# Optimization experiments

Hardware: AMD Instinct MI355X
Metric: run time of the kernel (lower is better)

Reference implementation:

```python
import jax, jax.numpy as jnp
import numpy as np

N_NODES = 100000
N_EDGES = 1600000
HIDDEN = 64
EPS = 1e-5


def setup_inputs() -> dict:
    key = jax.random.key(0)
    ks = jax.random.split(key, 12)
    h = HIDDEN
    inp = {
        'x': jax.random.normal(ks[0], (N_NODES, h), dtype=jnp.float32),
        'edge_index': jax.random.randint(ks[1], (2, N_EDGES), 0, N_NODES, dtype=jnp.int32),
        'message': jax.random.normal(ks[2], (N_EDGES, h), dtype=jnp.float32),
        # node_mlp: Linear(2h->h), BN(h), ReLU, Dropout(identity), Linear(h->h), BN(h), ReLU
        'W1': jax.random.normal(ks[3], (2 * h, h), dtype=jnp.float32) / np.sqrt(2.0 * h),
        'b1': jnp.zeros((h,), jnp.float32),
        'g1': jnp.ones((h,), jnp.float32),
        'be1': jnp.zeros((h,), jnp.float32),
        'W2': jax.random.normal(ks[4], (h, h), dtype=jnp.float32) / np.sqrt(h),
        'b2': jnp.zeros((h,), jnp.float32),
        'g2': jnp.ones((h,), jnp.float32),
        'be2': jnp.zeros((h,), jnp.float32),
        # attention_mlp: Linear(h->1), Sigmoid
        'Wa': jax.random.normal(ks[5], (h, 1), dtype=jnp.float32) / np.sqrt(h),
        'ba': jnp.zeros((1,), jnp.float32),
    }
    return inp


def _scatter_max(msg, idx, n):
    # torch_scatter scatter(..., reduce='max') fills segments with no edges with 0
    agg = jax.ops.segment_max(msg, idx, num_segments=n)  # [N, H], -inf where empty
    cnt = jax.ops.segment_sum(jnp.ones((idx.shape[0],), msg.dtype), idx, num_segments=n)
    return jnp.where(cnt[:, None] > 0, agg, jnp.zeros((), msg.dtype))


def _batchnorm(x, gamma, beta):
    # training-mode BatchNorm1d: batch mean / biased variance
    mu = jnp.mean(x, axis=0)
    var = jnp.mean((x - mu) ** 2, axis=0)
    return (x - mu) * jax.lax.rsqrt(var + EPS) * gamma + beta


def reference(x, edge_index, message, W1, b1, g1, be1, W2, b2, g2, be2, Wa, ba):
    n = x.shape[0]
    row, col = edge_index[0], edge_index[1]
    fwd = _scatter_max(message, col, n)   # [N, H]
    bwd = _scatter_max(message, row, n)   # [N, H]
    out = jnp.concatenate([fwd, bwd], axis=1)          # [N, 2H]
    h1 = jax.nn.relu(_batchnorm(out @ W1 + b1, g1, be1))  # dropout = identity (eval)
    h2 = jax.nn.relu(_batchnorm(h1 @ W2 + b2, g2, be2))   # [N, H]
    att = jax.nn.sigmoid(h2 @ Wa + ba).reshape(-1)          # [N]
    return (h2, att)
```

## Files before the change

kernel.cpp:

```cpp
#include <hip/hip_runtime.h>
#include <hip/hip_bf16.h>
#include <cstdint>
#include <cstddef>

#define HDIM 64
#define EPS 1e-5f
#define BN 64
#define BSH 6
#define LR 65
#define NXCD 8
#define BCAPX 256
#define SENTE 64u

typedef short bf16x8 __attribute__((ext_vector_type(8)));
typedef float f32x4  __attribute__((ext_vector_type(4)));
typedef float f4v    __attribute__((ext_vector_type(4)));
typedef unsigned u2v __attribute__((ext_vector_type(2)));

__device__ __forceinline__ unsigned bf16rn(float f) {
    unsigned u = __float_as_uint(f);
    return (u + 0x7FFFu + ((u >> 16) & 1u)) >> 16;
}

__global__ __launch_bounds__(256) void bucket_fill_kernel(
    const int* __restrict__ ei, unsigned* __restrict__ bcur,
    unsigned* __restrict__ entries, int E, int nblk) {
    int e = blockIdx.x * 256 + threadIdx.x;
    if (e >= E) return;
    unsigned xcd;
    asm volatile("s_getreg_b32 %0, hwreg(HW_REG_XCC_ID)" : "=s"(xcd));
    xcd &= (NXCD - 1);
    int row = ei[e];
    int col = ei[(size_t)E + e];
    unsigned cell1 = (unsigned)(col >> BSH) * NXCD + xcd;
    unsigned p1 = atomicAdd(&bcur[cell1], 1u);
    if (p1 < BCAPX)
        entries[(size_t)cell1 * BCAPX + p1] = ((unsigned)e << 7) | (unsigned)(col & (BN - 1));
    unsigned cell2 = (unsigned)(nblk + (row >> BSH)) * NXCD + xcd;
    unsigned p2 = atomicAdd(&bcur[cell2], 1u);
    if (p2 < BCAPX)
        entries[(size_t)cell2 * BCAPX + p2] = ((unsigned)e << 7) | (unsigned)(row & (BN - 1));
}

__global__ __launch_bounds__(256) void binned_max_kernel(
    const float* __restrict__ msg, const unsigned* __restrict__ bcur,
    const unsigned* __restrict__ entries,
    unsigned short* __restrict__ fwdB, unsigned short* __restrict__ bwdB,
    int N, int nblk) {
    __shared__ __align__(16) float acc[4 * LR * BN];
    int tid = threadIdx.x;
    int wave = tid >> 6, lane = tid & 63;
    int b = blockIdx.x;

    {
        f4v mi = { -INFINITY, -INFINITY, -INFINITY, -INFINITY };
        f4v* p = (f4v*)acc;
        for (int i = tid; i < 4 * LR * BN / 4; i += 256) p[i] = mi;
    }
    __syncthreads();
    float* accw = acc + wave * (LR * BN);

    for (int rr = 0; rr < 2; ++rr) {
        int r = wave + rr * 4;
        unsigned cnt = bcur[(size_t)b * NXCD + r];
        if (cnt > BCAPX) cnt = BCAPX;
        const unsigned* rb = entries + ((size_t)b * NXCD + r) * BCAPX;
        for (unsigned c0 = 0; c0 < cnt; c0 += 64) {
            unsigned myent = (c0 + (unsigned)lane < cnt) ? rb[c0 + lane] : SENTE;
            unsigned rem = cnt - c0;
#pragma unroll
            for (int b16 = 0; b16 < 4; ++b16) {
                if ((unsigned)(b16 * 16) >= rem) break;
                float v[16]; unsigned sl[16];
#pragma unroll
                for (int k = 0; k < 16; ++k) {
                    unsigned ent = __shfl(myent, b16 * 16 + k);
                    sl[k] = ent & 127u;
                    v[k] = __builtin_nontemporal_load(&msg[(size_t)(ent >> 7) * HDIM + lane]);
                }
#pragma unroll
                for (int k = 0; k < 16; ++k) {
                    float* a = &accw[sl[k] * BN + lane];
                    *a = fmaxf(*a, v[k]);
                }
            }
        }
    }
    __syncthreads();

    bool fwd = (b < nblk);
    int node0 = (fwd ? b : b - nblk) * BN;
    unsigned short* dst = fwd ? fwdB : bwdB;
    for (int i = tid; i < BN * (HDIM / 4); i += 256) {
        int rrow = i >> 4, c4 = (i & 15) * 4;
        int node = node0 + rrow;
        if (node >= N) continue;
        int off = rrow * HDIM + c4;
        f4v m0 = *(const f4v*)&acc[0 * LR * BN + off];
        f4v m1 = *(const f4v*)&acc[1 * LR * BN + off];
        f4v m2 = *(const f4v*)&acc[2 * LR * BN + off];
        f4v m3 = *(const f4v*)&acc[3 * LR * BN + off];
        f4v m;
#pragma unroll
        for (int k = 0; k < 4; ++k) {
            float x = fmaxf(fmaxf(m0[k], m1[k]), fmaxf(m2[k], m3[k]));
            m[k] = (x == -INFINITY) ? 0.0f : x;
        }
        u2v o;
        o.x = bf16rn(m[0]) | (bf16rn(m[1]) << 16);
        o.y = bf16rn(m[2]) | (bf16rn(m[3]) << 16);
        *(u2v*)(dst + (size_t)node * HDIM + c4) = o;
    }
}


__global__ __launch_bounds__(256) void prep_w_kernel(
    const float* __restrict__ W1, const float* __restrict__ W2,
    unsigned short* __restrict__ W1T, unsigned short* __restrict__ W2T) {
    int t = blockIdx.x * 256 + threadIdx.x;
    if (t < 128 * 64) {
        int k = t >> 6, o = t & 63;
        W1T[o * 128 + k] = (unsigned short)bf16rn(W1[t]);
    } else {
        int t2 = t - 128 * 64;
        if (t2 < 64 * 64) {
            int k = t2 >> 6, o = t2 & 63;
            W2T[o * 64 + k] = (unsigned short)bf16rn(W2[t2]);
        }
    }
}

__global__ __launch_bounds__(256) void gemm1_mfma_kernel(
    const unsigned short* __restrict__ fwdB, const unsigned short* __restrict__ bwdB,
    const unsigned short* __restrict__ W1T, const float* __restrict__ b1,
    float* __restrict__ y1, float* __restrict__ sum1, float* __restrict__ sq1, int N) {
    __shared__ float wsum[4][64], wsq[4][64];
    int tid = threadIdx.x;
    int wave = tid >> 6, lane = tid & 63;
    int lrow = lane & 15, kseg = lane >> 4;
    int rbase = blockIdx.x * 64 + wave * 16;

    bf16x8 bfr[4][4];
#pragma unroll
    for (int nt = 0; nt < 4; ++nt)
#pragma unroll
        for (int kb = 0; kb < 4; ++kb)
            bfr[nt][kb] = *(const bf16x8*)(W1T + (size_t)(nt * 16 + lrow) * 128 + kb * 32 + kseg * 8);

    int r = rbase + lrow;
    bool ok = (r < N);
    size_t ro = (size_t)(ok ? r : 0) * HDIM;
    bf16x8 z = {};
    bf16x8 afr[4];
    afr[0] = *(const bf16x8*)(fwdB + ro + kseg * 8);
    afr[1] = *(const bf16x8*)(fwdB + ro + 32 + kseg * 8);
    afr[2] = *(const bf16x8*)(bwdB + ro + kseg * 8);
    afr[3] = *(const bf16x8*)(bwdB + ro + 32 + kseg * 8);
    if (!ok) { afr[0] = z; afr[1] = z; afr[2] = z; afr[3] = z; }

    f32x4 acc[4] = {};
#pragma unroll
    for (int kb = 0; kb < 4; ++kb)
#pragma unroll
        for (int nt = 0; nt < 4; ++nt)
            acc[nt] = __builtin_amdgcn_mfma_f32_16x16x32_bf16(afr[kb], bfr[nt][kb], acc[nt], 0, 0, 0);

#pragma unroll
    for (int nt = 0; nt < 4; ++nt) {
        int col = nt * 16 + lrow;
        float bias = b1[col];
        float s = 0.f, q = 0.f;
#pragma unroll
        for (int rr = 0; rr < 4; ++rr) {
            int rowi = rbase + kseg * 4 + rr;
            if (rowi < N) {
                float v = acc[nt][rr] + bias;
                y1[(size_t)rowi * HDIM + col] = v;
                s += v; q += v * v;
            }
        }
        s += __shfl_xor(s, 16); s += __shfl_xor(s, 32);
        q += __shfl_xor(q, 16); q += __shfl_xor(q, 32);
        if (kseg == 0) { wsum[wave][col] = s; wsq[wave][col] = q; }
    }
    __syncthreads();
    if (tid < 64) {
        float S = wsum[0][tid] + wsum[1][tid] + wsum[2][tid] + wsum[3][tid];
        float Q = wsq[0][tid] + wsq[1][tid] + wsq[2][tid] + wsq[3][tid];
        atomicAdd(&sum1[tid], S);
        atomicAdd(&sq1[tid], Q);
    }
}

__global__ __launch_bounds__(256) void gemm2_mfma_kernel(
    const float* __restrict__ y1, const float* __restrict__ sum1, const float* __restrict__ sq1,
    const float* __restrict__ g1, const float* __restrict__ be1,
    const unsigned short* __restrict__ W2T, const float* __restrict__ b2,
    float* __restrict__ y2, float* __restrict__ sum2, float* __restrict__ sq2, int N) {
    __shared__ float sc[64], sh[64];
    __shared__ float wsum[4][64], wsq[4][64];
    int tid = threadIdx.x;
    if (tid < 64) {
        float invN = 1.0f / (float)N;
        float mu = sum1[tid] * invN;
        float var = sq1[tid] * invN - mu * mu;
        float rs = rsqrtf(var + EPS);
        float s = rs * g1[tid];
        sc[tid] = s;
        sh[tid] = be1[tid] - mu * s;
    }
    __syncthreads();
    int wave = tid >> 6, lane = tid & 63;
    int lrow = lane & 15, kseg = lane >> 4;
    int rbase = blockIdx.x * 64 + wave * 16;

    bf16x8 bfr[4][2];
#pragma unroll
    for (int nt = 0; nt < 4; ++nt)
#pragma unroll
        for (int kb = 0; kb < 2; ++kb)
            bfr[nt][kb] = *(const bf16x8*)(W2T + (size_t)(nt * 16 + lrow) * 64 + kb * 32 + kseg * 8);

    int r = rbase + lrow;
    size_t ro = (size_t)((r < N) ? r : 0) * HDIM;
    bf16x8 afr[2];
#pragma unroll
    for (int kb = 0; kb < 2; ++kb) {
        const f4v* yp = (const f4v*)(y1 + ro + kb * 32 + kseg * 8);
        f4v u0 = yp[0], u1 = yp[1];
        int k0 = kb * 32 + kseg * 8;
        bf16x8 a;
#pragma unroll
        for (int j = 0; j < 4; ++j) {
            float h0 = fmaxf(fmaf(u0[j], sc[k0 + j], sh[k0 + j]), 0.f);
            float h1 = fmaxf(fmaf(u1[j], sc[k0 + 4 + j], sh[k0 + 4 + j]), 0.f);
            a[j] = (short)bf16rn(h0);
            a[4 + j] = (short)bf16rn(h1);
        }
        afr[kb] = a;
    }

    f32x4 acc[4] = {};
#pragma unroll
    for (int kb = 0; kb < 2; ++kb)
#pragma unroll
        for (int nt = 0; nt < 4; ++nt)
            acc[nt] = __builtin_amdgcn_mfma_f32_16x16x32_bf16(afr[kb], bfr[nt][kb], acc[nt], 0, 0, 0);

#pragma unroll
    for (int nt = 0; nt < 4; ++nt) {
        int col = nt * 16 + lrow;
        float bias = b2[col];
        float s = 0.f, q = 0.f;
#pragma unroll
        for (int rr = 0; rr < 4; ++rr) {
            int rowi = rbase + kseg * 4 + rr;
            if (rowi < N) {
                float v = acc[nt][rr] + bias;
                y2[(size_t)rowi * HDIM + col] = v;
                s += v; q += v * v;
            }
        }
        s += __shfl_xor(s, 16); s += __shfl_xor(s, 32);
        q += __shfl_xor(q, 16); q += __shfl_xor(q, 32);
        if (kseg == 0) { wsum[wave][col] = s; wsq[wave][col] = q; }
    }
    __syncthreads();
    if (tid < 64) {
        float S = wsum[0][tid] + wsum[1][tid] + wsum[2][tid] + wsum[3][tid];
        float Q = wsq[0][tid] + wsq[1][tid] + wsq[2][tid] + wsq[3][tid];
        atomicAdd(&sum2[tid], S);
        atomicAdd(&sq2[tid], Q);
    }
}

__global__ __launch_bounds__(256) void final_kernel(
    const float* __restrict__ y2, const float* __restrict__ sum2, const float* __restrict__ sq2,
    const float* __restrict__ g2, const float* __restrict__ be2,
    const float* __restrict__ Wa, const float* __restrict__ ba,
    float* __restrict__ out_h2, float* __restrict__ out_att, int N) {
    __shared__ float sc[HDIM], sh[HDIM], wa[HDIM];
    __shared__ float bav;
    if (threadIdx.x < HDIM) {
        int c = threadIdx.x;
        float invN = 1.0f / (float)N;
        float mu = sum2[c] * invN;
        float var = sq2[c] * invN - mu * mu;
        float rstd = rsqrtf(var + EPS);
        float s = rstd * g2[c];
        sc[c] = s;
        sh[c] = be2[c] - mu * s;
        wa[c] = Wa[c];
    }
    if (threadIdx.x == 0) bav = ba[0];
    __syncthreads();
    int n = blockIdx.x * 256 + threadIdx.x;
    if (n >= N) return;

    const f4v* p = (const f4v*)&y2[(size_t)n * HDIM];
    f4v* dst = (f4v*)&out_h2[(size_t)n * HDIM];
    float att = bav;
#pragma unroll 1
    for (int kk = 0; kk < 16; ++kk) {
        f4v u = p[kk];
        f4v hv;
#pragma unroll
        for (int j = 0; j < 4; ++j) {
            int k = kk * 4 + j;
            float h = fmaxf(fmaf(u[j], sc[k], sh[k]), 0.0f);
            hv[j] = h;
            att = fmaf(h, wa[k], att);
        }
        dst[kk] = hv;
    }
    out_att[n] = 1.0f / (1.0f + expf(-att));
}

extern "C" void kernel_launch(void* const* d_in, const int* in_sizes, int n_in,
                              void* d_out, int out_size, void* d_ws, size_t ws_size,
                              hipStream_t stream) {
    const int*   ei   = (const int*)d_in[1];
    const float* msg  = (const float*)d_in[2];
    const float* W1   = (const float*)d_in[3];
    const float* b1   = (const float*)d_in[4];
    const float* g1   = (const float*)d_in[5];
    const float* be1  = (const float*)d_in[6];
    const float* W2   = (const float*)d_in[7];
    const float* b2   = (const float*)d_in[8];
    const float* g2   = (const float*)d_in[9];
    const float* be2  = (const float*)d_in[10];
    const float* Wa   = (const float*)d_in[11];
    const float* ba   = (const float*)d_in[12];

    const int N = in_sizes[0] / HDIM;
    const int E = in_sizes[1] / 2;
    const int nblk = (N + BN - 1) / BN;

    unsigned short* fwdB = (unsigned short*)d_ws;
    unsigned short* bwdB = fwdB + (size_t)N * HDIM;
    unsigned short* W1T  = bwdB + (size_t)N * HDIM;
    unsigned short* W2T  = W1T + 8192;
    float*    stats      = (float*)(W2T + 4096);
    unsigned* bcur       = (unsigned*)(stats + 256);
    unsigned* entries    = bcur + (size_t)2 * nblk * NXCD;
    float*    y1         = (float*)d_out;
    float*    y2         = (float*)d_ws;
    float*    out_att    = (float*)d_out + (size_t)N * HDIM;

    hipMemsetAsync(stats, 0, 256 * sizeof(float)
                             + (size_t)2 * nblk * NXCD * sizeof(unsigned), stream);
    prep_w_kernel<<<48, 256, 0, stream>>>(W1, W2, W1T, W2T);

    int eblocks = (E + 255) / 256;
    bucket_fill_kernel<<<eblocks, 256, 0, stream>>>(ei, bcur, entries, E, nblk);
    binned_max_kernel<<<2 * nblk, 256, 0, stream>>>(msg, bcur, entries, fwdB, bwdB, N, nblk);

    int G = (N + 63) / 64;
    gemm1_mfma_kernel<<<G, 256, 0, stream>>>(fwdB, bwdB, W1T, b1, y1,
                                             stats, stats + 64, N);
    gemm2_mfma_kernel<<<G, 256, 0, stream>>>(y1, stats, stats + 64, g1, be1,
                                             W2T, b2, y2, stats + 128, stats + 192, N);
    final_kernel<<<(N + 255) / 256, 256, 0, stream>>>(y2, stats + 128, stats + 192,
                                                      g2, be2, Wa, ba,
                                                      (float*)d_out, out_att, N);
}
```

Baseline: 535.1 us.

## Pad bucket counters to cache lines and prefetch next message batch in max kernel

Bucket counters are spaced 16 words apart so that atomics from different cells no longer land on the same cache line, and both atomics are issued before the entry stores. In the binned max kernel, the next 16 message rows are loaded while the current 16 are reduced into shared memory, so gather latency overlaps the LDS max work. The trade-off is a larger memset and counter footprint, plus higher register pressure from the double-buffered values, which could lower occupancy.

```diff
diff --git a/kernel.cpp b/kernel.cpp
--- a/kernel.cpp
+++ b/kernel.cpp
@@ -10,6 +10,7 @@
 #define LR 65
 #define NXCD 8
 #define BCAPX 256
+#define CURPAD 16
 #define SENTE 64u
 
 typedef short bf16x8 __attribute__((ext_vector_type(8)));
@@ -33,11 +34,11 @@
     int row = ei[e];
     int col = ei[(size_t)E + e];
     unsigned cell1 = (unsigned)(col >> BSH) * NXCD + xcd;
-    unsigned p1 = atomicAdd(&bcur[cell1], 1u);
+    unsigned cell2 = (unsigned)(nblk + (row >> BSH)) * NXCD + xcd;
+    unsigned p1 = atomicAdd(&bcur[(size_t)cell1 * CURPAD], 1u);
+    unsigned p2 = atomicAdd(&bcur[(size_t)cell2 * CURPAD], 1u);
     if (p1 < BCAPX)
         entries[(size_t)cell1 * BCAPX + p1] = ((unsigned)e << 7) | (unsigned)(col & (BN - 1));
-    unsigned cell2 = (unsigned)(nblk + (row >> BSH)) * NXCD + xcd;
-    unsigned p2 = atomicAdd(&bcur[cell2], 1u);
     if (p2 < BCAPX)
         entries[(size_t)cell2 * BCAPX + p2] = ((unsigned)e << 7) | (unsigned)(row & (BN - 1));
 }
@@ -62,26 +63,40 @@
 
     for (int rr = 0; rr < 2; ++rr) {
         int r = wave + rr * 4;
-        unsigned cnt = bcur[(size_t)b * NXCD + r];
+        unsigned cnt = bcur[((size_t)b * NXCD + r) * CURPAD];
         if (cnt > BCAPX) cnt = BCAPX;
         const unsigned* rb = entries + ((size_t)b * NXCD + r) * BCAPX;
         for (unsigned c0 = 0; c0 < cnt; c0 += 64) {
             unsigned myent = (c0 + (unsigned)lane < cnt) ? rb[c0 + lane] : SENTE;
             unsigned rem = cnt - c0;
+            float v[16];
+#pragma unroll
+            for (int k = 0; k < 16; ++k) {
+                unsigned ent = __shfl(myent, k);
+                v[k] = __builtin_nontemporal_load(&msg[(size_t)(ent >> 7) * HDIM + lane]);
+            }
 #pragma unroll
             for (int b16 = 0; b16 < 4; ++b16) {
                 if ((unsigned)(b16 * 16) >= rem) break;
-                float v[16]; unsigned sl[16];
+                bool more = (unsigned)((b16 + 1) * 16) < rem;
+                float vn[16];
+                if (more) {
+#pragma unroll
+                    for (int k = 0; k < 16; ++k) {
+                        unsigned ent = __shfl(myent, (b16 + 1) * 16 + k);
+                        vn[k] = __builtin_nontemporal_load(&msg[(size_t)(ent >> 7) * HDIM + lane]);
+                    }
+                }
 #pragma unroll
                 for (int k = 0; k < 16; ++k) {
                     unsigned ent = __shfl(myent, b16 * 16 + k);
-                    sl[k] = ent & 127u;
-                    v[k] = __builtin_nontemporal_load(&msg[(size_t)(ent >> 7) * HDIM + lane]);
+                    unsigned sl = ent & 127u;
+                    float* a = &accw[sl * BN + lane];
+                    *a = fmaxf(*a, v[k]);
                 }
-#pragma unroll
-                for (int k = 0; k < 16; ++k) {
-                    float* a = &accw[sl[k] * BN + lane];
-                    *a = fmaxf(*a, v[k]);
+                if (more) {
+#pragma unroll
+                    for (int k = 0; k < 16; ++k) v[k] = vn[k];
                 }
             }
         }
@@ -342,13 +357,13 @@
     unsigned short* W2T  = W1T + 8192;
     float*    stats      = (float*)(W2T + 4096);
     unsigned* bcur       = (unsigned*)(stats + 256);
-    unsigned* entries    = bcur + (size_t)2 * nblk * NXCD;
+    unsigned* entries    = bcur + (size_t)2 * nblk * NXCD * CURPAD;
     float*    y1         = (float*)d_out;
     float*    y2         = (float*)d_ws;
     float*    out_att    = (float*)d_out + (size_t)N * HDIM;
 
     hipMemsetAsync(stats, 0, 256 * sizeof(float)
-                             + (size_t)2 * nblk * NXCD * sizeof(unsigned), stream);
+                             + (size_t)2 * nblk * NXCD * CURPAD * sizeof(unsigned), stream);
     prep_w_kernel<<<48, 256, 0, stream>>>(W1, W2, W1T, W2T);
 
     int eblocks = (E + 255) / 256;
```

New measurement: 498.5 us. -6.8%, faster.
